# Kernel tuning notes

Hardware: AMD Instinct MI355X
Metric: run time of the kernel (lower is better)

The kernel has to match this reference:

```python
import jax, jax.numpy as jnp
import numpy as np

N, DEG = 50000, 48       # nodes, fixed neighbor-table degree (excl. self-loop)
DIN, DOUT, K = 128, 128, 32
TEMP = 1.0


def setup_inputs() -> dict:
    key = jax.random.key(0)
    k1, k2, k3, k4 = jax.random.split(key, 4)
    feat = jax.random.normal(k1, (N, DIN), dtype=jnp.float32)
    neighbors = jax.random.randint(k2, (N, DEG), 0, N)  # int neighbor ids
    edge_weight = jax.random.uniform(k3, (N, DEG), dtype=jnp.float32)
    limit = float(np.sqrt(6.0 / (DIN + DOUT)))  # Glorot uniform
    weight = jax.random.uniform(k4, (DIN, DOUT), dtype=jnp.float32, minval=-limit, maxval=limit)
    bias = jnp.zeros((DOUT,), dtype=jnp.float32)
    return {"feat": feat, "edge_weight": edge_weight, "weight": weight,
            "bias": bias, "neighbors": neighbors}


def _soft_k_conv(feat, edge_weight, weight, bias, neighbors):
    n = feat.shape[0]
    # linear transform first (as in module: feat = feat @ self.weight)
    x = feat @ weight                                        # [n, dout]
    # add self-loop edge with weight 1.0 (add_self_loop=True, norm='none')
    nb = jnp.concatenate([neighbors, jnp.arange(n)[:, None]], axis=1)      # [n, deg+1]
    w = jnp.concatenate([edge_weight, jnp.ones((n, 1), edge_weight.dtype)], axis=1)
    # top-k neighbors per row by edge weight (degree > k, so no -1 padding)
    tw, ti = jax.lax.top_k(w, K)                             # [n, k]
    idx = jnp.take_along_axis(nb, ti, axis=1)                # [n, k] neighbor ids
    xi = x[idx]                                              # [n, k, dout] gather
    # pairwise L2 distances within each top-k neighborhood via Gram trick
    sq = jnp.sum(xi * xi, axis=-1)                           # [n, k]
    gram = jnp.einsum('nkd,nld->nkl', xi, xi)                # [n, k, k]
    d2 = sq[:, :, None] + sq[:, None, :] - 2.0 * gram
    pos = d2 > 0
    dmat = jnp.where(pos, jnp.sqrt(jnp.where(pos, d2, 1.0)), 0.0)  # safe sqrt
    # weighted medoid distances: sum_b w[i,b] * D[i,a,b]
    dist = jnp.einsum('nl,nkl->nk', tw, dmat)                # [n, k]
    rel = jax.nn.softmax(-dist / TEMP, axis=-1)              # [n, k]
    # with_weight_correction=True
    rel = rel * tw
    rel = rel / jnp.sum(rel, axis=-1, keepdims=True)
    # softmax-weighted spmm aggregation over top-k neighbors
    out = jnp.einsum('nk,nkd->nd', rel, xi) + bias           # [n, dout]
    return out


def reference(feat, edge_weight, weight, bias, neighbors):
    return _soft_k_conv(feat, edge_weight, weight, bias, neighbors)
```

## Files before the change

### kernel.cpp

```cpp
#include <hip/hip_runtime.h>
#include <hip/hip_bf16.h>

#define NNODE_DIN 128
#define NNODE_DOUT 128
#define DEG 48
#define TOPK 32

typedef _Float16 halfx8 __attribute__((ext_vector_type(8)));
typedef unsigned short ushortx8 __attribute__((ext_vector_type(8)));
typedef float floatx4 __attribute__((ext_vector_type(4)));

__device__ inline unsigned short f2h(float f) {
    _Float16 h = (_Float16)f;
    return __builtin_bit_cast(unsigned short, h);
}
__device__ inline float h2f(unsigned short u) {
    return (float)__builtin_bit_cast(_Float16, u);
}
__device__ inline float fast_sqrt(float x) {
    float r; asm("v_sqrt_f32 %0, %1" : "=v"(r) : "v"(x)); return r;
}
__device__ inline float fast_exp(float x) {
    float t = x * 1.44269504088896341f;
    float r; asm("v_exp_f32 %0, %1" : "=v"(r) : "v"(t)); return r;
}
__device__ inline float fast_rcp(float x) {
    float r; asm("v_rcp_f32 %0, %1" : "=v"(r) : "v"(x)); return r;
}

__global__ __launch_bounds__(256) void k0_wprep(
    const float* __restrict__ w, unsigned short* __restrict__ wth,
    unsigned short* __restrict__ wtl) {
    int tid = blockIdx.x * 256 + threadIdx.x;
    int lane = tid & 63;
    int kt = (tid >> 6) & 3;
    int nt = tid >> 8;
    int m = lane & 15, q = lane >> 4;
    int nn = nt * 16 + m;
    int k0 = kt * 32 + q * 8;
    ushortx8 uh, ul;
#pragma unroll
    for (int e = 0; e < 8; ++e) {
        float v = w[(size_t)(k0 + e) * 128 + nn];
        unsigned short h = f2h(v);
        uh[e] = h;
        ul[e] = f2h(v - h2f(h));
    }
    *(ushortx8*)(wth + tid * 8) = uh;
    *(ushortx8*)(wtl + tid * 8) = ul;
}

__global__ __launch_bounds__(64, 4) void k1_mfma(
    const float* __restrict__ feat, const unsigned short* __restrict__ wth,
    const unsigned short* __restrict__ wtl, unsigned short* __restrict__ xf,
    int n) {
    __shared__ float s_x[16 * 132];
    int l = threadIdx.x;
    int m = l & 15, q = l >> 4;
    int r0 = blockIdx.x * 16;

    halfx8 ah[4], al[4];
#pragma unroll
    for (int kt = 0; kt < 4; ++kt) {
        float vv[8];
        if (r0 + m < n) {
            const float* src = feat + (size_t)(r0 + m) * 128 + kt * 32 + q * 8;
            float4 v0 = *(const float4*)src;
            float4 v1 = *(const float4*)(src + 4);
            vv[0] = v0.x; vv[1] = v0.y; vv[2] = v0.z; vv[3] = v0.w;
            vv[4] = v1.x; vv[5] = v1.y; vv[6] = v1.z; vv[7] = v1.w;
        } else {
#pragma unroll
            for (int e = 0; e < 8; ++e) vv[e] = 0.0f;
        }
        ushortx8 uh, ul;
#pragma unroll
        for (int e = 0; e < 8; ++e) {
            unsigned short h = f2h(vv[e]);
            uh[e] = h;
            ul[e] = f2h(vv[e] - h2f(h));
        }
        ah[kt] = __builtin_bit_cast(halfx8, uh);
        al[kt] = __builtin_bit_cast(halfx8, ul);
    }

#pragma unroll 2
    for (int nt = 0; nt < 8; ++nt) {
        floatx4 a = (floatx4){0.f, 0.f, 0.f, 0.f};
#pragma unroll
        for (int kt = 0; kt < 4; ++kt) {
            int fo = ((nt * 4 + kt) * 64 + l) * 8;
            halfx8 bh = *(const halfx8*)(wth + fo);
            halfx8 bl = *(const halfx8*)(wtl + fo);
            a = __builtin_amdgcn_mfma_f32_16x16x32_f16(ah[kt], bh, a, 0, 0, 0);
            a = __builtin_amdgcn_mfma_f32_16x16x32_f16(ah[kt], bl, a, 0, 0, 0);
            a = __builtin_amdgcn_mfma_f32_16x16x32_f16(al[kt], bh, a, 0, 0, 0);
        }
#pragma unroll
        for (int r = 0; r < 4; ++r)
            s_x[(q * 4 + r) * 132 + nt * 16 + m] = a[r];
    }
    __syncthreads();

#pragma unroll
    for (int rr = 0; rr < 2; ++rr) {
        int row = rr * 8 + (l >> 3);
        int c0 = (l & 7) * 16;
        if (r0 + row < n) {
            float vv[16];
#pragma unroll
            for (int j = 0; j < 4; ++j) {
                float4 v = *(const float4*)&s_x[row * 132 + c0 + j * 4];
                vv[j * 4 + 0] = v.x; vv[j * 4 + 1] = v.y;
                vv[j * 4 + 2] = v.z; vv[j * 4 + 3] = v.w;
            }
            unsigned u[8];
#pragma unroll
            for (int p = 0; p < 8; ++p) {
                u[p] = (unsigned)f2h(vv[2 * p]) | ((unsigned)f2h(vv[2 * p + 1]) << 16);
            }
            size_t off = (size_t)(r0 + row) * 128 + c0;
            *(uint4*)(xf + off) = make_uint4(u[0], u[1], u[2], u[3]);
            *(uint4*)(xf + off + 8) = make_uint4(u[4], u[5], u[6], u[7]);
        }
    }
}

__global__ __launch_bounds__(64, 4) void k2_conv(
    const float* __restrict__ ew, const int* __restrict__ nbr,
    const float* __restrict__ bias, const unsigned short* __restrict__ xf,
    float* __restrict__ outp, int n) {
    __shared__ float s_w[52];
    __shared__ int s_nb[52];
    __shared__ float s_tw[32];
    __shared__ int s_id[32];
    __shared__ float s_diag[32];
    __shared__ float s_dist[32];
    __shared__ float s_omega[32];
    __shared__ _Float16 s_rows[32][128];

    int i = blockIdx.x;
    int l = threadIdx.x;

    if (l < DEG + 1) {
        bool self = (l == DEG);
        s_w[l] = self ? 1.0f : ew[(size_t)i * DEG + l];
        s_nb[l] = self ? i : nbr[(size_t)i * DEG + l];
    }
    __syncthreads();

    if (l < DEG + 1) {
        float wj = s_w[l];
        int rank = 0;
#pragma unroll
        for (int t2 = 0; t2 < DEG + 1; ++t2) {
            float wt = s_w[t2];
            rank += (wt > wj) || ((wt == wj) && (t2 < l)) ? 1 : 0;
        }
        if (rank < TOPK) {
            s_tw[rank] = wj;
            s_id[rank] = s_nb[l];
        }
    }
    __syncthreads();

    int m = l & 15;
    int q = l >> 4;
    int row0 = s_id[m];
    int row1 = s_id[16 + m];
    const _Float16* g0 = (const _Float16*)xf + (size_t)row0 * 128 + q * 8;
    const _Float16* g1 = (const _Float16*)xf + (size_t)row1 * 128 + q * 8;

    halfx8 H0[4], H1[4];
#pragma unroll
    for (int kt = 0; kt < 4; ++kt) {
        H0[kt] = *(const halfx8*)(g0 + kt * 32);
        H1[kt] = *(const halfx8*)(g1 + kt * 32);
    }
#pragma unroll
    for (int kt = 0; kt < 4; ++kt) {
        *(halfx8*)&s_rows[m][kt * 32 + q * 8] = H0[kt];
        *(halfx8*)&s_rows[16 + m][kt * 32 + q * 8] = H1[kt];
    }

    floatx4 acc[2][2];
#pragma unroll
    for (int a = 0; a < 2; ++a)
#pragma unroll
        for (int b = 0; b < 2; ++b) acc[a][b] = (floatx4){0.f, 0.f, 0.f, 0.f};

#pragma unroll
    for (int kt = 0; kt < 4; ++kt) {
        halfx8 h0 = H0[kt], h1 = H1[kt];
        acc[0][0] = __builtin_amdgcn_mfma_f32_16x16x32_f16(h0, h0, acc[0][0], 0, 0, 0);
        acc[0][1] = __builtin_amdgcn_mfma_f32_16x16x32_f16(h0, h1, acc[0][1], 0, 0, 0);
        acc[1][0] = __builtin_amdgcn_mfma_f32_16x16x32_f16(h1, h0, acc[1][0], 0, 0, 0);
        acc[1][1] = __builtin_amdgcn_mfma_f32_16x16x32_f16(h1, h1, acc[1][1], 0, 0, 0);
    }

    if (q == (m >> 2)) {
        int rd = m & 3;
        s_diag[m] = acc[0][0][rd];
        s_diag[16 + m] = acc[1][1][rd];
    }
    __syncthreads();

    {
        float db0 = s_diag[m];
        float db1 = s_diag[16 + m];
        float tw0 = s_tw[m];
        float tw1 = s_tw[16 + m];
#pragma unroll
        for (int ma = 0; ma < 2; ++ma) {
#pragma unroll
            for (int r = 0; r < 4; ++r) {
                int a = ma * 16 + q * 4 + r;
                float da = s_diag[a];
                float g0v = acc[ma][0][r];
                float g1v = acc[ma][1][r];
                float d20 = da + db0 - 2.0f * g0v;
                float d21 = da + db1 - 2.0f * g1v;
                float t0 = (d20 > 0.0f) ? fast_sqrt(d20) : 0.0f;
                float t1 = (d21 > 0.0f) ? fast_sqrt(d21) : 0.0f;
                float v = tw0 * t0 + tw1 * t1;
                v += __shfl_xor(v, 1);
                v += __shfl_xor(v, 2);
                v += __shfl_xor(v, 4);
                v += __shfl_xor(v, 8);
                if (m == 0) s_dist[a] = v;
            }
        }
    }
    __syncthreads();

    {
        int k32 = l & 31;
        float s = s_dist[k32];
        float mn = s;
        mn = fminf(mn, __shfl_xor(mn, 1));
        mn = fminf(mn, __shfl_xor(mn, 2));
        mn = fminf(mn, __shfl_xor(mn, 4));
        mn = fminf(mn, __shfl_xor(mn, 8));
        mn = fminf(mn, __shfl_xor(mn, 16));
        float e = fast_exp(mn - s) * s_tw[k32];
        float sum = e;
        sum += __shfl_xor(sum, 1);
        sum += __shfl_xor(sum, 2);
        sum += __shfl_xor(sum, 4);
        sum += __shfl_xor(sum, 8);
        sum += __shfl_xor(sum, 16);
        float om = e * fast_rcp(sum);
        if (l < 32) s_omega[l] = om;
    }
    __syncthreads();

    {
        int d0 = 2 * l;
        float2 bb = *(const float2*)(bias + d0);
        float o0 = bb.x, o1 = bb.y;
#pragma unroll
        for (int b = 0; b < 32; ++b) {
            float wb = s_omega[b];
            unsigned uu = *(const unsigned*)&s_rows[b][d0];
            o0 += wb * h2f((unsigned short)(uu & 0xffff));
            o1 += wb * h2f((unsigned short)(uu >> 16));
        }
        *(float2*)(outp + (size_t)i * 128 + d0) = make_float2(o0, o1);
    }
}

extern "C" void kernel_launch(void* const* d_in, const int* in_sizes, int n_in,
                              void* d_out, int out_size, void* d_ws, size_t ws_size,
                              hipStream_t stream) {
    const float* feat = (const float*)d_in[0];
    const float* ew = (const float*)d_in[1];
    const float* weight = (const float*)d_in[2];
    const float* bias = (const float*)d_in[3];
    const int* nbr = (const int*)d_in[4];
    float* outp = (float*)d_out;
    int n = in_sizes[0] / NNODE_DIN;

    unsigned short* xf = (unsigned short*)d_ws;
    unsigned short* wth = xf + (size_t)n * NNODE_DOUT;
    unsigned short* wtl = wth + 2048 * 8;

    hipLaunchKernelGGL(k0_wprep, dim3(8), dim3(256), 0, stream, weight, wth, wtl);
    int grid1 = (n + 15) / 16;
    hipLaunchKernelGGL(k1_mfma, dim3(grid1), dim3(64), 0, stream, feat, wth, wtl, xf, n);
    hipLaunchKernelGGL(k2_conv, dim3(n), dim3(64), 0, stream, ew, nbr, bias, xf, outp, n);
}
```

Measured before the change: 200.6 us.

## Split k1 GEMM output tiles across four waves and pad k2 shared rows

The projection kernel now runs 256 threads per block, with each of four waves computing two of the eight 16-column output tiles instead of one wave doing all eight. The fp16 pack-and-store epilogue is spread across all 256 threads. Separately, the shared-memory row buffer in the conv kernel is padded from 128 to 136 halves to reduce LDS bank conflicts. Each wave in k1 still converts the full 16-row A fragment redundantly, and the larger block may lower how many blocks fit per CU.

```diff
diff --git a/kernel.cpp b/kernel.cpp
--- a/kernel.cpp
+++ b/kernel.cpp
@@ -50,12 +50,14 @@
     *(ushortx8*)(wtl + tid * 8) = ul;
 }
 
-__global__ __launch_bounds__(64, 4) void k1_mfma(
+__global__ __launch_bounds__(256, 4) void k1_mfma(
     const float* __restrict__ feat, const unsigned short* __restrict__ wth,
     const unsigned short* __restrict__ wtl, unsigned short* __restrict__ xf,
     int n) {
     __shared__ float s_x[16 * 132];
-    int l = threadIdx.x;
+    int t = threadIdx.x;
+    int w = t >> 6;
+    int l = t & 63;
     int m = l & 15, q = l >> 4;
     int r0 = blockIdx.x * 16;
 
@@ -84,8 +86,9 @@
         al[kt] = __builtin_bit_cast(halfx8, ul);
     }
 
-#pragma unroll 2
-    for (int nt = 0; nt < 8; ++nt) {
+#pragma unroll
+    for (int nn = 0; nn < 2; ++nn) {
+        int nt = 2 * w + nn;
         floatx4 a = (floatx4){0.f, 0.f, 0.f, 0.f};
 #pragma unroll
         for (int kt = 0; kt < 4; ++kt) {
@@ -102,26 +105,18 @@
     }
     __syncthreads();
 
-#pragma unroll
-    for (int rr = 0; rr < 2; ++rr) {
-        int row = rr * 8 + (l >> 3);
-        int c0 = (l & 7) * 16;
+    {
+        int row = t >> 4;
+        int c0 = (t & 15) * 8;
         if (r0 + row < n) {
-            float vv[16];
-#pragma unroll
-            for (int j = 0; j < 4; ++j) {
-                float4 v = *(const float4*)&s_x[row * 132 + c0 + j * 4];
-                vv[j * 4 + 0] = v.x; vv[j * 4 + 1] = v.y;
-                vv[j * 4 + 2] = v.z; vv[j * 4 + 3] = v.w;
-            }
-            unsigned u[8];
-#pragma unroll
-            for (int p = 0; p < 8; ++p) {
-                u[p] = (unsigned)f2h(vv[2 * p]) | ((unsigned)f2h(vv[2 * p + 1]) << 16);
-            }
+            float4 v0 = *(const float4*)&s_x[row * 132 + c0];
+            float4 v1 = *(const float4*)&s_x[row * 132 + c0 + 4];
+            unsigned u0 = (unsigned)f2h(v0.x) | ((unsigned)f2h(v0.y) << 16);
+            unsigned u1 = (unsigned)f2h(v0.z) | ((unsigned)f2h(v0.w) << 16);
+            unsigned u2 = (unsigned)f2h(v1.x) | ((unsigned)f2h(v1.y) << 16);
+            unsigned u3 = (unsigned)f2h(v1.z) | ((unsigned)f2h(v1.w) << 16);
             size_t off = (size_t)(r0 + row) * 128 + c0;
-            *(uint4*)(xf + off) = make_uint4(u[0], u[1], u[2], u[3]);
-            *(uint4*)(xf + off + 8) = make_uint4(u[4], u[5], u[6], u[7]);
+            *(uint4*)(xf + off) = make_uint4(u0, u1, u2, u3);
         }
     }
 }
@@ -137,7 +132,7 @@
     __shared__ float s_diag[32];
     __shared__ float s_dist[32];
     __shared__ float s_omega[32];
-    __shared__ _Float16 s_rows[32][128];
+    __shared__ _Float16 s_rows[32][136];
 
     int i = blockIdx.x;
     int l = threadIdx.x;
@@ -286,6 +281,6 @@
 
     hipLaunchKernelGGL(k0_wprep, dim3(8), dim3(256), 0, stream, weight, wth, wtl);
     int grid1 = (n + 15) / 16;
-    hipLaunchKernelGGL(k1_mfma, dim3(grid1), dim3(64), 0, stream, feat, wth, wtl, xf, n);
+    hipLaunchKernelGGL(k1_mfma, dim3(grid1), dim3(256), 0, stream, feat, wth, wtl, xf, n);
     hipLaunchKernelGGL(k2_conv, dim3(n), dim3(64), 0, stream, ew, nbr, bias, xf, outp, n);
 }
```

After: 191.8 us. -4.4%, faster.

## Split per-node conv work across two wavefronts with shared-memory row exchange

Applied to the files above, without the earlier changes.

The per-node conv kernel now uses 128 threads (two wavefronts) instead of one. Each wave gathers 16 of the 32 top-k rows, stages them in padded shared memory, and reads the other wave's rows back to compute its half of the Gram matrix with two MFMAs instead of four. The final aggregation gives each thread one output column. This doubles wave-level parallelism per node and halves per-wave gather and MFMA work, at the cost of an extra barrier and LDS round-trip, and the softmax step runs on only one wave.

```diff
diff --git a/kernel.cpp b/kernel.cpp
--- a/kernel.cpp
+++ b/kernel.cpp
@@ -126,7 +126,7 @@
     }
 }
 
-__global__ __launch_bounds__(64, 4) void k2_conv(
+__global__ __launch_bounds__(128, 4) void k2_conv(
     const float* __restrict__ ew, const int* __restrict__ nbr,
     const float* __restrict__ bias, const unsigned short* __restrict__ xf,
     float* __restrict__ outp, int n) {
@@ -137,103 +137,92 @@
     __shared__ float s_diag[32];
     __shared__ float s_dist[32];
     __shared__ float s_omega[32];
-    __shared__ _Float16 s_rows[32][128];
+    __shared__ _Float16 s_rows[32][136];
 
     int i = blockIdx.x;
-    int l = threadIdx.x;
-
-    if (l < DEG + 1) {
-        bool self = (l == DEG);
-        s_w[l] = self ? 1.0f : ew[(size_t)i * DEG + l];
-        s_nb[l] = self ? i : nbr[(size_t)i * DEG + l];
-    }
-    __syncthreads();
-
-    if (l < DEG + 1) {
-        float wj = s_w[l];
+    int t = threadIdx.x;
+    int w = t >> 6;
+    int l = t & 63;
+
+    if (t < DEG + 1) {
+        bool self = (t == DEG);
+        s_w[t] = self ? 1.0f : ew[(size_t)i * DEG + t];
+        s_nb[t] = self ? i : nbr[(size_t)i * DEG + t];
+    }
+    __syncthreads();
+
+    if (t < DEG + 1) {
+        float wj = s_w[t];
         int rank = 0;
 #pragma unroll
         for (int t2 = 0; t2 < DEG + 1; ++t2) {
             float wt = s_w[t2];
-            rank += (wt > wj) || ((wt == wj) && (t2 < l)) ? 1 : 0;
+            rank += (wt > wj) || ((wt == wj) && (t2 < t)) ? 1 : 0;
         }
         if (rank < TOPK) {
             s_tw[rank] = wj;
-            s_id[rank] = s_nb[l];
+            s_id[rank] = s_nb[t];
         }
     }
     __syncthreads();
 
     int m = l & 15;
     int q = l >> 4;
-    int row0 = s_id[m];
-    int row1 = s_id[16 + m];
-    const _Float16* g0 = (const _Float16*)xf + (size_t)row0 * 128 + q * 8;
-    const _Float16* g1 = (const _Float16*)xf + (size_t)row1 * 128 + q * 8;
-
-    halfx8 H0[4], H1[4];
+    int a0 = w * 16;
+    int o0 = 16 - a0;
+    int rowg = s_id[a0 + m];
+    const _Float16* gp = (const _Float16*)xf + (size_t)rowg * 128 + q * 8;
+
+    halfx8 Hown[4];
+#pragma unroll
+    for (int kt = 0; kt < 4; ++kt) Hown[kt] = *(const halfx8*)(gp + kt * 32);
+#pragma unroll
+    for (int kt = 0; kt < 4; ++kt)
+        *(halfx8*)&s_rows[a0 + m][kt * 32 + q * 8] = Hown[kt];
+    __syncthreads();
+
+    halfx8 Hoth[4];
+#pragma unroll
+    for (int kt = 0; kt < 4; ++kt)
+        Hoth[kt] = *(const halfx8*)&s_rows[o0 + m][kt * 32 + q * 8];
+
+    floatx4 accO = (floatx4){0.f, 0.f, 0.f, 0.f};
+    floatx4 accX = (floatx4){0.f, 0.f, 0.f, 0.f};
 #pragma unroll
     for (int kt = 0; kt < 4; ++kt) {
-        H0[kt] = *(const halfx8*)(g0 + kt * 32);
-        H1[kt] = *(const halfx8*)(g1 + kt * 32);
-    }
-#pragma unroll
-    for (int kt = 0; kt < 4; ++kt) {
-        *(halfx8*)&s_rows[m][kt * 32 + q * 8] = H0[kt];
-        *(halfx8*)&s_rows[16 + m][kt * 32 + q * 8] = H1[kt];
-    }
-
-    floatx4 acc[2][2];
-#pragma unroll
-    for (int a = 0; a < 2; ++a)
-#pragma unroll
-        for (int b = 0; b < 2; ++b) acc[a][b] = (floatx4){0.f, 0.f, 0.f, 0.f};
-
-#pragma unroll
-    for (int kt = 0; kt < 4; ++kt) {
-        halfx8 h0 = H0[kt], h1 = H1[kt];
-        acc[0][0] = __builtin_amdgcn_mfma_f32_16x16x32_f16(h0, h0, acc[0][0], 0, 0, 0);
-        acc[0][1] = __builtin_amdgcn_mfma_f32_16x16x32_f16(h0, h1, acc[0][1], 0, 0, 0);
-        acc[1][0] = __builtin_amdgcn_mfma_f32_16x16x32_f16(h1, h0, acc[1][0], 0, 0, 0);
-        acc[1][1] = __builtin_amdgcn_mfma_f32_16x16x32_f16(h1, h1, acc[1][1], 0, 0, 0);
+        accO = __builtin_amdgcn_mfma_f32_16x16x32_f16(Hown[kt], Hown[kt], accO, 0, 0, 0);
+        accX = __builtin_amdgcn_mfma_f32_16x16x32_f16(Hown[kt], Hoth[kt], accX, 0, 0, 0);
     }
 
     if (q == (m >> 2)) {
-        int rd = m & 3;
-        s_diag[m] = acc[0][0][rd];
-        s_diag[16 + m] = acc[1][1][rd];
+        s_diag[a0 + m] = accO[m & 3];
     }
     __syncthreads();
 
     {
-        float db0 = s_diag[m];
-        float db1 = s_diag[16 + m];
-        float tw0 = s_tw[m];
-        float tw1 = s_tw[16 + m];
-#pragma unroll
-        for (int ma = 0; ma < 2; ++ma) {
-#pragma unroll
-            for (int r = 0; r < 4; ++r) {
-                int a = ma * 16 + q * 4 + r;
-                float da = s_diag[a];
-                float g0v = acc[ma][0][r];
-                float g1v = acc[ma][1][r];
-                float d20 = da + db0 - 2.0f * g0v;
-                float d21 = da + db1 - 2.0f * g1v;
-                float t0 = (d20 > 0.0f) ? fast_sqrt(d20) : 0.0f;
-                float t1 = (d21 > 0.0f) ? fast_sqrt(d21) : 0.0f;
-                float v = tw0 * t0 + tw1 * t1;
-                v += __shfl_xor(v, 1);
-                v += __shfl_xor(v, 2);
-                v += __shfl_xor(v, 4);
-                v += __shfl_xor(v, 8);
-                if (m == 0) s_dist[a] = v;
-            }
-        }
-    }
-    __syncthreads();
-
-    {
+        float dbO = s_diag[a0 + m];
+        float dbX = s_diag[o0 + m];
+        float twO = s_tw[a0 + m];
+        float twX = s_tw[o0 + m];
+#pragma unroll
+        for (int r = 0; r < 4; ++r) {
+            int a = a0 + q * 4 + r;
+            float da = s_diag[a];
+            float d2o = da + dbO - 2.0f * accO[r];
+            float d2x = da + dbX - 2.0f * accX[r];
+            float t0 = (d2o > 0.0f) ? fast_sqrt(d2o) : 0.0f;
+            float t1 = (d2x > 0.0f) ? fast_sqrt(d2x) : 0.0f;
+            float v = twO * t0 + twX * t1;
+            v += __shfl_xor(v, 1);
+            v += __shfl_xor(v, 2);
+            v += __shfl_xor(v, 4);
+            v += __shfl_xor(v, 8);
+            if (m == 0) s_dist[a] = v;
+        }
+    }
+    __syncthreads();
+
+    if (w == 0) {
         int k32 = l & 31;
         float s = s_dist[k32];
         float mn = s;
@@ -255,17 +244,12 @@
     __syncthreads();
 
     {
-        int d0 = 2 * l;
-        float2 bb = *(const float2*)(bias + d0);
-        float o0 = bb.x, o1 = bb.y;
+        float o = bias[t];
 #pragma unroll
         for (int b = 0; b < 32; ++b) {
-            float wb = s_omega[b];
-            unsigned uu = *(const unsigned*)&s_rows[b][d0];
-            o0 += wb * h2f((unsigned short)(uu & 0xffff));
-            o1 += wb * h2f((unsigned short)(uu >> 16));
-        }
-        *(float2*)(outp + (size_t)i * 128 + d0) = make_float2(o0, o1);
+            o += s_omega[b] * (float)s_rows[b][t];
+        }
+        outp[(size_t)i * 128 + t] = o;
     }
 }
 
@@ -287,5 +271,5 @@
     hipLaunchKernelGGL(k0_wprep, dim3(8), dim3(256), 0, stream, weight, wth, wtl);
     int grid1 = (n + 15) / 16;
     hipLaunchKernelGGL(k1_mfma, dim3(grid1), dim3(64), 0, stream, feat, wth, wtl, xf, n);
-    hipLaunchKernelGGL(k2_conv, dim3(n), dim3(64), 0, stream, ew, nbr, bias, xf, outp, n);
-}
+    hipLaunchKernelGGL(k2_conv, dim3(n), dim3(128), 0, stream, ew, nbr, bias, xf, outp, n);
+}
```

New measurement: 176.7 us. -11.9%, faster.
